# Kernel tuning notes

Hardware: AMD Instinct MI355X
Metric: run time of the kernel (lower is better)

## Reference

```python
import jax, jax.numpy as jnp
import numpy as np

B, S, E, H = 4, 2048, 1024, 16
HD = E // H

def setup_inputs() -> dict:
    key = jax.random.key(0)
    ks = jax.random.split(key, 11)
    scale = 1.0 / np.sqrt(E)
    inp = {
        'query': jax.random.normal(ks[0], (B, S, E), jnp.float32),
        'key':   jax.random.normal(ks[1], (B, S, E), jnp.float32),
        'value': jax.random.normal(ks[2], (B, S, E), jnp.float32),
        'Wq': jax.random.normal(ks[3], (E, E), jnp.float32) * scale,
        'bq': jax.random.normal(ks[4], (E,), jnp.float32) * scale,
        'Wk': jax.random.normal(ks[5], (E, E), jnp.float32) * scale,
        'bk': jax.random.normal(ks[6], (E,), jnp.float32) * scale,
        'Wv': jax.random.normal(ks[7], (E, E), jnp.float32) * scale,
        'bv': jax.random.normal(ks[8], (E,), jnp.float32) * scale,
        'Wo': jax.random.normal(ks[9], (E, E), jnp.float32) * scale,
        'bo': jax.random.normal(ks[10], (E,), jnp.float32) * scale,
    }
    return inp

def reference(query, key, value, Wq, bq, Wk, bk, Wv, bv, Wo, bo):
    # project and split heads: [B,S,E] -> [B,H,S,HD]
    def split_heads(x, W, b):
        y = jnp.einsum('bse,ef->bsf', x, W) + b
        return y.reshape(B, S, H, HD).transpose(0, 2, 1, 3)
    q = split_heads(query, Wq, bq)
    k = split_heads(key, Wk, bk)
    v = split_heads(value, Wv, bv)
    # scaled dot-product attention (dropout in eval mode -> identity)
    score = jnp.einsum('bhqd,bhkd->bhqk', q, k) / jnp.sqrt(jnp.float32(HD))
    p_attn = jax.nn.softmax(score, axis=-1)
    x = jnp.einsum('bhqk,bhkd->bhqd', p_attn, v)
    x = x.transpose(0, 2, 1, 3).reshape(B, S, E)
    return jnp.einsum('bse,ef->bsf', x, Wo) + bo
```

## Files before the change

### kernel.cpp

```cpp
#include <hip/hip_runtime.h>
#include <math.h>

typedef unsigned short ushort_t;
typedef unsigned int uint_t;
typedef short short8 __attribute__((ext_vector_type(8)));
typedef float float4a __attribute__((ext_vector_type(4)));
typedef uint_t uint4a __attribute__((ext_vector_type(4)));
typedef uint_t uint2a __attribute__((ext_vector_type(2)));

#define B_SZ 4
#define S_SZ 2048
#define E_SZ 1024
#define H_SZ 16
#define HD_SZ 64

#if __has_builtin(__builtin_amdgcn_exp2f)
#define EXP2F(x) __builtin_amdgcn_exp2f(x)
#else
#define EXP2F(x) exp2f(x)
#endif

__device__ __forceinline__ ushort_t f2bf(float f) {
    uint_t u = __builtin_bit_cast(uint_t, f);
    u = (u + 0x7fff + ((u >> 16) & 1)) >> 16;
    return (ushort_t)u;
}
__device__ __forceinline__ uint_t pk_bf16(float a, float b) {
    uint_t ua = __builtin_bit_cast(uint_t, a) + 0x8000u;
    uint_t ub = __builtin_bit_cast(uint_t, b) + 0x8000u;
#if __has_builtin(__builtin_amdgcn_perm)
    return __builtin_amdgcn_perm(ub, ua, 0x07060302u);
#else
    return (ua >> 16) | (ub & 0xffff0000u);
#endif
}
__device__ __forceinline__ void async_copy16(const void* g, void* l) {
    __builtin_amdgcn_global_load_lds(
        (const __attribute__((address_space(1))) void*)g,
        (__attribute__((address_space(3))) void*)l, 16, 0, 0);
}

__global__ __launch_bounds__(256) void transpose4(
    const float* __restrict__ W0, const float* __restrict__ W1,
    const float* __restrict__ W2, const float* __restrict__ W3,
    ushort_t* __restrict__ out)
{
    const float* src;
    switch (blockIdx.z) {
        case 0: src = W0; break;
        case 1: src = W1; break;
        case 2: src = W2; break;
        default: src = W3; break;
    }
    ushort_t* dst = out + (size_t)blockIdx.z * (E_SZ * E_SZ);
    __shared__ ushort_t t[32][33];
    int x = blockIdx.x * 32 + threadIdx.x;
    int y0 = blockIdx.y * 32;
    for (int i = threadIdx.y; i < 32; i += 8)
        t[i][threadIdx.x] = f2bf(src[(size_t)(y0 + i) * E_SZ + x]);
    __syncthreads();
    int yy = blockIdx.x * 32;
    int xx = y0 + threadIdx.x;
    for (int i = threadIdx.y; i < 32; i += 8)
        dst[(size_t)(yy + i) * E_SZ + xx] = t[threadIdx.x][i];
}

__global__ __launch_bounds__(256) void cvt3(
    const float* __restrict__ s0, const float* __restrict__ s1,
    const float* __restrict__ s2, ushort_t* __restrict__ d0,
    ushort_t* __restrict__ d1, ushort_t* __restrict__ d2)
{
    const float* s; ushort_t* d;
    switch (blockIdx.y) {
        case 0: s = s0; d = d0; break;
        case 1: s = s1; d = d1; break;
        default: s = s2; d = d2; break;
    }
    size_t i = ((size_t)blockIdx.x * 256 + threadIdx.x) * 8;
    float4a u0 = *(const float4a*)(s + i);
    float4a u1 = *(const float4a*)(s + i + 4);
    uint4a w = (uint4a){pk_bf16(u0[0], u0[1]), pk_bf16(u0[2], u0[3]),
                        pk_bf16(u1[0], u1[1]), pk_bf16(u1[2], u1[3])};
    *(uint4a*)(d + i) = w;
}

template<bool OUTF32>
__device__ __forceinline__ void gemm_body(
    const ushort_t* X, const ushort_t* Wt, const float* bias,
    void* Yv, int mode, int tileM, int tileN)
{
    __shared__ __align__(16) ushort_t As[4][4096];
    __shared__ __align__(16) ushort_t Bs[4][4096];
    const int tid = threadIdx.x;
    const int lane = tid & 63;
    const int quad = lane >> 4;
    const int l15 = lane & 15;
    const int wid = tid >> 6;
    const int wm = (wid >> 1) * 64;
    const int wn = (wid & 1) * 64;

    float4a acc[4][4];
    #pragma unroll
    for (int i = 0; i < 4; i++)
        #pragma unroll
        for (int j = 0; j < 4; j++)
            acc[i][j] = (float4a){0.f, 0.f, 0.f, 0.f};

    const ushort_t* pA0 = X  + (size_t)(tileM + (tid & 127)) * E_SZ + (tid >> 7) * 8;
    const ushort_t* pA1 = X  + (size_t)(tileM + (tid & 127)) * E_SZ + ((tid >> 7) + 2) * 8;
    const ushort_t* pB0 = Wt + (size_t)(tileN + (tid & 127)) * E_SZ + (tid >> 7) * 8;
    const ushort_t* pB1 = Wt + (size_t)(tileN + (tid & 127)) * E_SZ + ((tid >> 7) + 2) * 8;
    const int d0 = tid * 8;
    const int d1 = (256 + tid) * 8;

#define STAGE(SLOT) do { \
    async_copy16(pA0, &As[SLOT][d0]); \
    async_copy16(pA1, &As[SLOT][d1]); \
    async_copy16(pB0, &Bs[SLOT][d0]); \
    async_copy16(pB1, &Bs[SLOT][d1]); \
    pA0 += 32; pA1 += 32; pB0 += 32; pB1 += 32; } while (0)

    STAGE(0); STAGE(1); STAGE(2);

#define KTILE(SLOT, DOSTAGE, VMS) do { \
    asm volatile("s_waitcnt lgkmcnt(0)" ::: "memory"); \
    __builtin_amdgcn_s_barrier(); \
    asm volatile("" ::: "memory"); \
    if (DOSTAGE) STAGE(((SLOT) + 3) & 3); \
    asm volatile("s_waitcnt vmcnt(" #VMS ")" ::: "memory"); \
    __builtin_amdgcn_s_barrier(); \
    asm volatile("" ::: "memory"); \
    { \
        short8 a[4], b[4]; \
        _Pragma("unroll") \
        for (int mt = 0; mt < 4; mt++) \
            a[mt] = *(const short8*)&As[SLOT][quad * 1024 + (wm + mt * 16 + l15) * 8]; \
        _Pragma("unroll") \
        for (int nt = 0; nt < 4; nt++) \
            b[nt] = *(const short8*)&Bs[SLOT][quad * 1024 + (wn + nt * 16 + l15) * 8]; \
        __builtin_amdgcn_s_setprio(1); \
        _Pragma("unroll") \
        for (int mt = 0; mt < 4; mt++) \
            _Pragma("unroll") \
            for (int nt = 0; nt < 4; nt++) \
                acc[mt][nt] = __builtin_amdgcn_mfma_f32_16x16x32_bf16( \
                    a[mt], b[nt], acc[mt][nt], 0, 0, 0); \
        __builtin_amdgcn_s_setprio(0); \
    } } while (0)

    #pragma unroll 1
    for (int j = 0; j < 28; j += 4) {
        KTILE(0, true, 12);
        KTILE(1, true, 12);
        KTILE(2, true, 12);
        KTILE(3, true, 12);
    }
    KTILE(0, true, 12);
    KTILE(1, false, 8);
    KTILE(2, false, 4);
    KTILE(3, false, 0);
#undef KTILE
#undef STAGE

    #pragma unroll
    for (int nt = 0; nt < 4; nt++) {
        int n = tileN + wn + nt * 16 + l15;
        float bv = bias[n];
        #pragma unroll
        for (int mt = 0; mt < 4; mt++) {
            #pragma unroll
            for (int r = 0; r < 4; r++) {
                int m = tileM + wm + mt * 16 + quad * 4 + r;
                float v = acc[mt][nt][r] + bv;
                if constexpr (OUTF32) {
                    ((float*)Yv)[(size_t)m * E_SZ + n] = v;
                } else {
                    ushort_t* Y = (ushort_t*)Yv;
                    if (mode == 0) {
                        Y[(size_t)m * E_SZ + n] = f2bf(v);
                    } else {
                        int bb = m >> 11, s = m & 2047;
                        Y[((size_t)(bb * E_SZ + n)) * S_SZ + s] = f2bf(v);
                    }
                }
            }
        }
    }
}

__global__ __launch_bounds__(256, 2) void proj3(
    const ushort_t* __restrict__ x0, const ushort_t* __restrict__ x1,
    const ushort_t* __restrict__ x2, const ushort_t* __restrict__ Wt,
    const float* __restrict__ b0, const float* __restrict__ b1,
    const float* __restrict__ b2, ushort_t* __restrict__ y0,
    ushort_t* __restrict__ y1, ushort_t* __restrict__ y2)
{
    const ushort_t* X; const float* bias; ushort_t* Y; int mode = 0;
    switch (blockIdx.z) {
        case 0: X = x0; bias = b0; Y = y0; break;
        case 1: X = x1; bias = b1; Y = y1; break;
        default: X = x2; bias = b2; Y = y2; mode = 1; break;
    }
    gemm_body<false>(X, Wt + (size_t)blockIdx.z * E_SZ * E_SZ, bias, Y, mode,
                     blockIdx.y * 128, blockIdx.x * 128);
}

__global__ __launch_bounds__(256, 2) void gemm_out(
    const ushort_t* __restrict__ X, const ushort_t* __restrict__ Wt,
    const float* __restrict__ bias, float* __restrict__ Y)
{
    gemm_body<true>(X, Wt, bias, Y, 0, blockIdx.y * 128, blockIdx.x * 128);
}

__global__ __launch_bounds__(256) void attn(
    const ushort_t* __restrict__ Q, const ushort_t* __restrict__ K,
    const ushort_t* __restrict__ V, ushort_t* __restrict__ ctx)
{
    __shared__ __align__(16) ushort_t smem[32768];
    ushort_t* PQ = smem;
    ushort_t* Ks = smem + 16384;
    ushort_t* Vt = smem + 24576;

    const int tid = threadIdx.x;
    const int lane = tid & 63;
    const int quad = lane >> 4;
    const int l15 = lane & 15;
    const int wid = tid >> 6;
    const int qt = blockIdx.x;
    const int bh = blockIdx.y;
    const int b = bh >> 4, h = bh & 15;
    const int s0 = qt * 128;
    const int wq = wid * 32;
    const float CE = 0.18033688011f;

    for (int p = 0; p < 4; p++) {
        int L = p * 256 + tid;
        int g = L >> 7, r = L & 127;
        const ushort_t* src = Q + ((size_t)(b * S_SZ + s0 + r)) * E_SZ + h * HD_SZ + g * 8;
        async_copy16(src, &PQ[L * 8]);
    }

    float4a st[8][2];
    float4a o[4][2];
    for (int mt = 0; mt < 4; mt++)
        for (int nt = 0; nt < 2; nt++)
            o[mt][nt] = (float4a){0.f, 0.f, 0.f, 0.f};
    float mrow[2] = {-1e30f, -1e30f};
    float lrow[2] = {0.f, 0.f};
    short8 qf[2][2];

    for (int kt = 0; kt < 16; kt++) {
        for (int p = 0; p < 4; p++) {
            int L = p * 256 + tid;
            int g = L >> 7, r = L & 127;
            const ushort_t* src = K + ((size_t)(b * S_SZ + kt * 128 + r)) * E_SZ + h * HD_SZ + g * 8;
            async_copy16(src, &Ks[L * 8]);
        }
        for (int p = 0; p < 4; p++) {
            int c = p * 256 + tid;
            int d = c >> 4, cc = c & 15;
            const ushort_t* src = V + ((size_t)(b * E_SZ + h * HD_SZ + d)) * S_SZ + kt * 128 + cc * 8;
            short8 val = *(const short8*)src;
            *(short8*)&Vt[d * 128 + ((cc ^ (d & 7)) << 3)] = val;
        }
        __syncthreads();
        if (kt == 0) {
            for (int ks = 0; ks < 2; ks++)
                for (int nt = 0; nt < 2; nt++)
                    qf[ks][nt] = *(const short8*)&PQ[(ks * 4 + quad) * 1024 + (wq + nt * 16 + l15) * 8];
            __syncthreads();
        }

        for (int mt = 0; mt < 8; mt++)
            for (int nt = 0; nt < 2; nt++)
                st[mt][nt] = (float4a){0.f, 0.f, 0.f, 0.f};
        for (int ks = 0; ks < 2; ks++) {
            for (int mt = 0; mt < 8; mt++) {
                short8 kf = *(const short8*)&Ks[(ks * 4 + quad) * 1024 + (mt * 16 + l15) * 8];
                for (int nt = 0; nt < 2; nt++)
                    st[mt][nt] = __builtin_amdgcn_mfma_f32_16x16x32_bf16(
                        kf, qf[ks][nt], st[mt][nt], 0, 0, 0);
            }
        }

        float rmax[2] = {-1e30f, -1e30f};
        for (int mt = 0; mt < 8; mt++)
            for (int nt = 0; nt < 2; nt++)
                for (int r = 0; r < 4; r++)
                    rmax[nt] = fmaxf(rmax[nt], st[mt][nt][r]);
        for (int nt = 0; nt < 2; nt++) {
            rmax[nt] = fmaxf(rmax[nt], __shfl_xor(rmax[nt], 16));
            rmax[nt] = fmaxf(rmax[nt], __shfl_xor(rmax[nt], 32));
        }
        float alpha[2], mc[2], rsum[2] = {0.f, 0.f};
        for (int nt = 0; nt < 2; nt++) {
            float mn = fmaxf(mrow[nt], rmax[nt]);
            alpha[nt] = EXP2F((mrow[nt] - mn) * CE);
            mrow[nt] = mn;
            mc[nt] = mn * CE;
        }
        for (int mt = 0; mt < 8; mt++)
            for (int nt = 0; nt < 2; nt++) {
                float e0 = EXP2F(fmaf(st[mt][nt][0], CE, -mc[nt]));
                float e1 = EXP2F(fmaf(st[mt][nt][1], CE, -mc[nt]));
                float e2 = EXP2F(fmaf(st[mt][nt][2], CE, -mc[nt]));
                float e3 = EXP2F(fmaf(st[mt][nt][3], CE, -mc[nt]));
                rsum[nt] += (e0 + e1) + (e2 + e3);
                uint2a pp = (uint2a){pk_bf16(e0, e1), pk_bf16(e2, e3)};
                int row = wq + nt * 16 + l15;
                *(uint2a*)&PQ[row * 128 + (((2 * mt + (quad >> 1)) ^ (row & 7)) << 3) + (quad & 1) * 4] = pp;
            }
        for (int nt = 0; nt < 2; nt++) {
            rsum[nt] += __shfl_xor(rsum[nt], 16);
            rsum[nt] += __shfl_xor(rsum[nt], 32);
            lrow[nt] = lrow[nt] * alpha[nt] + rsum[nt];
        }
        for (int mt = 0; mt < 4; mt++)
            for (int nt = 0; nt < 2; nt++)
                for (int r = 0; r < 4; r++)
                    o[mt][nt][r] *= alpha[nt];

        for (int kk = 0; kk < 4; kk++) {
            int swz = ((kk * 4 + quad) ^ (l15 & 7)) << 3;
            short8 a[4], pb[2];
            for (int mt = 0; mt < 4; mt++)
                a[mt] = *(const short8*)&Vt[(mt * 16 + l15) * 128 + swz];
            for (int nt = 0; nt < 2; nt++)
                pb[nt] = *(const short8*)&PQ[(wq + nt * 16 + l15) * 128 + swz];
            for (int mt = 0; mt < 4; mt++)
                for (int nt = 0; nt < 2; nt++)
                    o[mt][nt] = __builtin_amdgcn_mfma_f32_16x16x32_bf16(
                        a[mt], pb[nt], o[mt][nt], 0, 0, 0);
        }
        __syncthreads();
    }

    for (int nt = 0; nt < 2; nt++) {
        float inv = 1.f / lrow[nt];
        int s = s0 + wq + nt * 16 + l15;
        size_t base = ((size_t)(b * S_SZ + s)) * E_SZ + h * HD_SZ;
        for (int mt = 0; mt < 4; mt++) {
            int d = mt * 16 + quad * 4;
            uint2a w = (uint2a){pk_bf16(o[mt][nt][0] * inv, o[mt][nt][1] * inv),
                                pk_bf16(o[mt][nt][2] * inv, o[mt][nt][3] * inv)};
            *(uint2a*)&ctx[base + d] = w;
        }
    }
}

extern "C" void kernel_launch(void* const* d_in, const int* in_sizes, int n_in,
                              void* d_out, int out_size, void* d_ws, size_t ws_size,
                              hipStream_t stream) {
    const float* q_in = (const float*)d_in[0];
    const float* k_in = (const float*)d_in[1];
    const float* v_in = (const float*)d_in[2];
    const float* Wq = (const float*)d_in[3];
    const float* bq = (const float*)d_in[4];
    const float* Wk = (const float*)d_in[5];
    const float* bk = (const float*)d_in[6];
    const float* Wv = (const float*)d_in[7];
    const float* bv = (const float*)d_in[8];
    const float* Wo = (const float*)d_in[9];
    const float* bo = (const float*)d_in[10];

    ushort_t* ws = (ushort_t*)d_ws;
    const size_t WMAT = (size_t)E_SZ * E_SZ;
    const size_t TEN = (size_t)B_SZ * S_SZ * E_SZ;
    ushort_t* Wt = ws;
    ushort_t* qb = ws + 4 * WMAT;
    ushort_t* kb = qb + TEN;
    ushort_t* vb = kb + TEN;
    ushort_t* qp = vb + TEN;
    ushort_t* kp = qp + TEN;
    ushort_t* vp = kp + TEN;
    ushort_t* cx = qb;

    transpose4<<<dim3(32, 32, 4), dim3(32, 8), 0, stream>>>(Wq, Wk, Wv, Wo, Wt);
    cvt3<<<dim3(4096, 3), 256, 0, stream>>>(q_in, k_in, v_in, qb, kb, vb);
    proj3<<<dim3(8, 64, 3), 256, 0, stream>>>(qb, kb, vb, Wt, bq, bk, bv, qp, kp, vp);
    attn<<<dim3(16, 64), 256, 0, stream>>>(qp, kp, vp, cx);
    gemm_out<<<dim3(8, 64), 256, 0, stream>>>(cx, Wt + 3 * WMAT, bo, (float*)d_out);
}
```

Before: 458.4 us.

## Shrink attention LDS, interleave softmax with PV MFMAs, lazy max rescale

```diff
diff --git a/kernel.cpp b/kernel.cpp
--- a/kernel.cpp
+++ b/kernel.cpp
@@ -216,10 +216,11 @@
     const ushort_t* __restrict__ Q, const ushort_t* __restrict__ K,
     const ushort_t* __restrict__ V, ushort_t* __restrict__ ctx)
 {
-    __shared__ __align__(16) ushort_t smem[32768];
-    ushort_t* PQ = smem;
-    ushort_t* Ks = smem + 16384;
-    ushort_t* Vt = smem + 24576;
+    __shared__ __align__(16) ushort_t smem[20480];
+    ushort_t* Ks = smem;
+    ushort_t* Vt = smem + 8192;
+    ushort_t* Ps = smem + 16384;
+    ushort_t* Qs = smem + 8192;
 
     const int tid = threadIdx.x;
     const int lane = tid & 63;
@@ -237,8 +238,14 @@
         int L = p * 256 + tid;
         int g = L >> 7, r = L & 127;
         const ushort_t* src = Q + ((size_t)(b * S_SZ + s0 + r)) * E_SZ + h * HD_SZ + g * 8;
-        async_copy16(src, &PQ[L * 8]);
-    }
+        async_copy16(src, &Qs[L * 8]);
+    }
+    __syncthreads();
+    short8 qf[2][2];
+    for (int ks = 0; ks < 2; ks++)
+        for (int nt = 0; nt < 2; nt++)
+            qf[ks][nt] = *(const short8*)&Qs[(ks * 4 + quad) * 1024 + (wq + nt * 16 + l15) * 8];
+    __syncthreads();
 
     float4a st[8][2];
     float4a o[4][2];
@@ -247,7 +254,6 @@
             o[mt][nt] = (float4a){0.f, 0.f, 0.f, 0.f};
     float mrow[2] = {-1e30f, -1e30f};
     float lrow[2] = {0.f, 0.f};
-    short8 qf[2][2];
 
     for (int kt = 0; kt < 16; kt++) {
         for (int p = 0; p < 4; p++) {
@@ -264,16 +270,11 @@
             *(short8*)&Vt[d * 128 + ((cc ^ (d & 7)) << 3)] = val;
         }
         __syncthreads();
-        if (kt == 0) {
-            for (int ks = 0; ks < 2; ks++)
-                for (int nt = 0; nt < 2; nt++)
-                    qf[ks][nt] = *(const short8*)&PQ[(ks * 4 + quad) * 1024 + (wq + nt * 16 + l15) * 8];
-            __syncthreads();
-        }
 
         for (int mt = 0; mt < 8; mt++)
             for (int nt = 0; nt < 2; nt++)
                 st[mt][nt] = (float4a){0.f, 0.f, 0.f, 0.f};
+        __builtin_amdgcn_s_setprio(1);
         for (int ks = 0; ks < 2; ks++) {
             for (int mt = 0; mt < 8; mt++) {
                 short8 kf = *(const short8*)&Ks[(ks * 4 + quad) * 1024 + (mt * 16 + l15) * 8];
@@ -282,55 +283,69 @@
                         kf, qf[ks][nt], st[mt][nt], 0, 0, 0);
             }
         }
+        __builtin_amdgcn_s_setprio(0);
 
         float rmax[2] = {-1e30f, -1e30f};
         for (int mt = 0; mt < 8; mt++)
-            for (int nt = 0; nt < 2; nt++)
-                for (int r = 0; r < 4; r++)
-                    rmax[nt] = fmaxf(rmax[nt], st[mt][nt][r]);
+            for (int nt = 0; nt < 2; nt++) {
+                rmax[nt] = fmaxf(fmaxf(rmax[nt], st[mt][nt][0]), st[mt][nt][1]);
+                rmax[nt] = fmaxf(fmaxf(rmax[nt], st[mt][nt][2]), st[mt][nt][3]);
+            }
         for (int nt = 0; nt < 2; nt++) {
             rmax[nt] = fmaxf(rmax[nt], __shfl_xor(rmax[nt], 16));
             rmax[nt] = fmaxf(rmax[nt], __shfl_xor(rmax[nt], 32));
         }
-        float alpha[2], mc[2], rsum[2] = {0.f, 0.f};
-        for (int nt = 0; nt < 2; nt++) {
-            float mn = fmaxf(mrow[nt], rmax[nt]);
-            alpha[nt] = EXP2F((mrow[nt] - mn) * CE);
-            mrow[nt] = mn;
-            mc[nt] = mn * CE;
-        }
-        for (int mt = 0; mt < 8; mt++)
+        float alpha[2] = {1.f, 1.f};
+        int grew = !__all((rmax[0] - mrow[0] <= 44.0f) &&
+                          (rmax[1] - mrow[1] <= 44.0f));
+        if (grew) {
+            float nm0 = fmaxf(mrow[0], rmax[0]);
+            float nm1 = fmaxf(mrow[1], rmax[1]);
+            alpha[0] = EXP2F((mrow[0] - nm0) * CE);
+            alpha[1] = EXP2F((mrow[1] - nm1) * CE);
+            mrow[0] = nm0; mrow[1] = nm1;
+            for (int mt = 0; mt < 4; mt++)
+                for (int nt = 0; nt < 2; nt++)
+                    for (int r = 0; r < 4; r++)
+                        o[mt][nt][r] *= alpha[nt];
+        }
+        float mc[2] = {mrow[0] * CE, mrow[1] * CE};
+        float rsum[2] = {0.f, 0.f};
+
+        for (int kk = 0; kk < 4; kk++) {
+            for (int mtL = 0; mtL < 2; mtL++) {
+                int mt = kk * 2 + mtL;
+                for (int nt = 0; nt < 2; nt++) {
+                    float e0 = EXP2F(fmaf(st[mt][nt][0], CE, -mc[nt]));
+                    float e1 = EXP2F(fmaf(st[mt][nt][1], CE, -mc[nt]));
+                    float e2 = EXP2F(fmaf(st[mt][nt][2], CE, -mc[nt]));
+                    float e3 = EXP2F(fmaf(st[mt][nt][3], CE, -mc[nt]));
+                    rsum[nt] += (e0 + e1) + (e2 + e3);
+                    uint2a pp = (uint2a){pk_bf16(e0, e1), pk_bf16(e2, e3)};
+                    int row = wq + nt * 16 + l15;
+                    int ch = (mtL * 2 + (quad >> 1)) ^ (row & 3);
+                    *(uint2a*)&Ps[row * 32 + ch * 8 + (quad & 1) * 4] = pp;
+                }
+            }
+            int swzV = ((kk * 4 + quad) ^ (l15 & 7)) << 3;
+            short8 a[4], pb[2];
+            for (int mt = 0; mt < 4; mt++)
+                a[mt] = *(const short8*)&Vt[(mt * 16 + l15) * 128 + swzV];
             for (int nt = 0; nt < 2; nt++) {
-                float e0 = EXP2F(fmaf(st[mt][nt][0], CE, -mc[nt]));
-                float e1 = EXP2F(fmaf(st[mt][nt][1], CE, -mc[nt]));
-                float e2 = EXP2F(fmaf(st[mt][nt][2], CE, -mc[nt]));
-                float e3 = EXP2F(fmaf(st[mt][nt][3], CE, -mc[nt]));
-                rsum[nt] += (e0 + e1) + (e2 + e3);
-                uint2a pp = (uint2a){pk_bf16(e0, e1), pk_bf16(e2, e3)};
                 int row = wq + nt * 16 + l15;
-                *(uint2a*)&PQ[row * 128 + (((2 * mt + (quad >> 1)) ^ (row & 7)) << 3) + (quad & 1) * 4] = pp;
-            }
+                pb[nt] = *(const short8*)&Ps[row * 32 + ((quad ^ (row & 3)) << 3)];
+            }
+            __builtin_amdgcn_s_setprio(1);
+            for (int mt = 0; mt < 4; mt++)
+                for (int nt = 0; nt < 2; nt++)
+                    o[mt][nt] = __builtin_amdgcn_mfma_f32_16x16x32_bf16(
+                        a[mt], pb[nt], o[mt][nt], 0, 0, 0);
+            __builtin_amdgcn_s_setprio(0);
+        }
         for (int nt = 0; nt < 2; nt++) {
             rsum[nt] += __shfl_xor(rsum[nt], 16);
             rsum[nt] += __shfl_xor(rsum[nt], 32);
             lrow[nt] = lrow[nt] * alpha[nt] + rsum[nt];
-        }
-        for (int mt = 0; mt < 4; mt++)
-            for (int nt = 0; nt < 2; nt++)
-                for (int r = 0; r < 4; r++)
-                    o[mt][nt][r] *= alpha[nt];
-
-        for (int kk = 0; kk < 4; kk++) {
-            int swz = ((kk * 4 + quad) ^ (l15 & 7)) << 3;
-            short8 a[4], pb[2];
-            for (int mt = 0; mt < 4; mt++)
-                a[mt] = *(const short8*)&Vt[(mt * 16 + l15) * 128 + swz];
-            for (int nt = 0; nt < 2; nt++)
-                pb[nt] = *(const short8*)&PQ[(wq + nt * 16 + l15) * 128 + swz];
-            for (int mt = 0; mt < 4; mt++)
-                for (int nt = 0; nt < 2; nt++)
-                    o[mt][nt] = __builtin_amdgcn_mfma_f32_16x16x32_bf16(
-                        a[mt], pb[nt], o[mt][nt], 0, 0, 0);
         }
         __syncthreads();
     }
```

Result: slower. 468.8 us (+2.3%).

## Lazy softmax rescale, hoisted load addressing, and MFMA priority hints in attention

Applied to the files above, without the earlier changes.

```diff
diff --git a/kernel.cpp b/kernel.cpp
--- a/kernel.cpp
+++ b/kernel.cpp
@@ -240,6 +240,13 @@
         async_copy16(src, &PQ[L * 8]);
     }
 
+    const ushort_t* kBase = K + ((size_t)(b * S_SZ + (tid & 127))) * E_SZ
+                              + h * HD_SZ + (tid >> 7) * 8;
+    const ushort_t* vBase = V + ((size_t)(b * E_SZ + h * HD_SZ + (tid >> 4))) * S_SZ
+                              + (tid & 15) * 8;
+    const int kDst = tid * 8;
+    const int vDst = (tid >> 4) * 128 + (((tid & 15) ^ ((tid >> 4) & 7)) << 3);
+
     float4a st[8][2];
     float4a o[4][2];
     for (int mt = 0; mt < 4; mt++)
@@ -250,19 +257,16 @@
     short8 qf[2][2];
 
     for (int kt = 0; kt < 16; kt++) {
+        #pragma unroll
+        for (int p = 0; p < 4; p++)
+            async_copy16(kBase + p * 16, &Ks[kDst + p * 2048]);
+        #pragma unroll
         for (int p = 0; p < 4; p++) {
-            int L = p * 256 + tid;
-            int g = L >> 7, r = L & 127;
-            const ushort_t* src = K + ((size_t)(b * S_SZ + kt * 128 + r)) * E_SZ + h * HD_SZ + g * 8;
-            async_copy16(src, &Ks[L * 8]);
-        }
-        for (int p = 0; p < 4; p++) {
-            int c = p * 256 + tid;
-            int d = c >> 4, cc = c & 15;
-            const ushort_t* src = V + ((size_t)(b * E_SZ + h * HD_SZ + d)) * S_SZ + kt * 128 + cc * 8;
-            short8 val = *(const short8*)src;
-            *(short8*)&Vt[d * 128 + ((cc ^ (d & 7)) << 3)] = val;
-        }
+            short8 val = *(const short8*)(vBase + (size_t)p * (16 * S_SZ));
+            *(short8*)&Vt[vDst + p * 2048] = val;
+        }
+        kBase += 128 * E_SZ;
+        vBase += 128;
         __syncthreads();
         if (kt == 0) {
             for (int ks = 0; ks < 2; ks++)
@@ -271,34 +275,55 @@
             __syncthreads();
         }
 
-        for (int mt = 0; mt < 8; mt++)
-            for (int nt = 0; nt < 2; nt++)
-                st[mt][nt] = (float4a){0.f, 0.f, 0.f, 0.f};
-        for (int ks = 0; ks < 2; ks++) {
+        __builtin_amdgcn_s_setprio(1);
+        {
+            const float4a z4 = (float4a){0.f, 0.f, 0.f, 0.f};
+            #pragma unroll
             for (int mt = 0; mt < 8; mt++) {
-                short8 kf = *(const short8*)&Ks[(ks * 4 + quad) * 1024 + (mt * 16 + l15) * 8];
+                short8 kf = *(const short8*)&Ks[quad * 1024 + (mt * 16 + l15) * 8];
+                #pragma unroll
                 for (int nt = 0; nt < 2; nt++)
                     st[mt][nt] = __builtin_amdgcn_mfma_f32_16x16x32_bf16(
-                        kf, qf[ks][nt], st[mt][nt], 0, 0, 0);
+                        kf, qf[0][nt], z4, 0, 0, 0);
             }
-        }
+            #pragma unroll
+            for (int mt = 0; mt < 8; mt++) {
+                short8 kf = *(const short8*)&Ks[(4 + quad) * 1024 + (mt * 16 + l15) * 8];
+                #pragma unroll
+                for (int nt = 0; nt < 2; nt++)
+                    st[mt][nt] = __builtin_amdgcn_mfma_f32_16x16x32_bf16(
+                        kf, qf[1][nt], st[mt][nt], 0, 0, 0);
+            }
+        }
+        __builtin_amdgcn_s_setprio(0);
 
         float rmax[2] = {-1e30f, -1e30f};
         for (int mt = 0; mt < 8; mt++)
-            for (int nt = 0; nt < 2; nt++)
-                for (int r = 0; r < 4; r++)
-                    rmax[nt] = fmaxf(rmax[nt], st[mt][nt][r]);
+            for (int nt = 0; nt < 2; nt++) {
+                rmax[nt] = fmaxf(fmaxf(rmax[nt], st[mt][nt][0]), st[mt][nt][1]);
+                rmax[nt] = fmaxf(fmaxf(rmax[nt], st[mt][nt][2]), st[mt][nt][3]);
+            }
         for (int nt = 0; nt < 2; nt++) {
             rmax[nt] = fmaxf(rmax[nt], __shfl_xor(rmax[nt], 16));
             rmax[nt] = fmaxf(rmax[nt], __shfl_xor(rmax[nt], 32));
         }
-        float alpha[2], mc[2], rsum[2] = {0.f, 0.f};
-        for (int nt = 0; nt < 2; nt++) {
-            float mn = fmaxf(mrow[nt], rmax[nt]);
-            alpha[nt] = EXP2F((mrow[nt] - mn) * CE);
-            mrow[nt] = mn;
-            mc[nt] = mn * CE;
-        }
+        float alpha[2] = {1.f, 1.f};
+        int grew = !__all((rmax[0] - mrow[0] <= 44.0f) &&
+                          (rmax[1] - mrow[1] <= 44.0f));
+        if (grew) {
+            float nm0 = fmaxf(mrow[0], rmax[0]);
+            float nm1 = fmaxf(mrow[1], rmax[1]);
+            alpha[0] = EXP2F((mrow[0] - nm0) * CE);
+            alpha[1] = EXP2F((mrow[1] - nm1) * CE);
+            mrow[0] = nm0; mrow[1] = nm1;
+            for (int mt = 0; mt < 4; mt++)
+                for (int nt = 0; nt < 2; nt++)
+                    for (int r = 0; r < 4; r++)
+                        o[mt][nt][r] *= alpha[nt];
+        }
+        float mc[2] = {mrow[0] * CE, mrow[1] * CE};
+        float rsum[2] = {0.f, 0.f};
+
         for (int mt = 0; mt < 8; mt++)
             for (int nt = 0; nt < 2; nt++) {
                 float e0 = EXP2F(fmaf(st[mt][nt][0], CE, -mc[nt]));
@@ -315,10 +340,6 @@
             rsum[nt] += __shfl_xor(rsum[nt], 32);
             lrow[nt] = lrow[nt] * alpha[nt] + rsum[nt];
         }
-        for (int mt = 0; mt < 4; mt++)
-            for (int nt = 0; nt < 2; nt++)
-                for (int r = 0; r < 4; r++)
-                    o[mt][nt][r] *= alpha[nt];
 
         for (int kk = 0; kk < 4; kk++) {
             int swz = ((kk * 4 + quad) ^ (l15 & 7)) << 3;
@@ -327,10 +348,12 @@
                 a[mt] = *(const short8*)&Vt[(mt * 16 + l15) * 128 + swz];
             for (int nt = 0; nt < 2; nt++)
                 pb[nt] = *(const short8*)&PQ[(wq + nt * 16 + l15) * 128 + swz];
+            __builtin_amdgcn_s_setprio(1);
             for (int mt = 0; mt < 4; mt++)
                 for (int nt = 0; nt < 2; nt++)
                     o[mt][nt] = __builtin_amdgcn_mfma_f32_16x16x32_bf16(
                         a[mt], pb[nt], o[mt][nt], 0, 0, 0);
+            __builtin_amdgcn_s_setprio(0);
         }
         __syncthreads();
     }
```

Result: no change. 461.5 us (+0.7%).
